# Kernel tuning notes

Hardware: AMD Instinct MI355X
Metric: run time of the kernel (lower is better)

## Reference

```python
import jax, jax.numpy as jnp
import numpy as np

LRELU = 0.2


def _gru(x, Wi, Wh, bi, bh):
    # x: [B,T,D]; Wi: [3H,D]; Wh: [3H,H]; PyTorch GRU equations.
    B, T, D = x.shape
    H = Wh.shape[1]
    xW = jnp.einsum('btd,gd->btg', x, Wi) + bi  # precompute input projections
    def step(h, xw):
        gh = h @ Wh.T + bh
        xr, xz, xn = jnp.split(xw, 3, axis=-1)
        hr, hz, hn = jnp.split(gh, 3, axis=-1)
        r = jax.nn.sigmoid(xr + hr)
        z = jax.nn.sigmoid(xz + hz)
        n = jnp.tanh(xn + r * hn)
        h_new = (1.0 - z) * n + z * h
        return h_new, h_new
    h0 = jnp.zeros((B, H), x.dtype)
    hT, hs = jax.lax.scan(step, h0, jnp.swapaxes(xW, 0, 1))
    return jnp.swapaxes(hs, 0, 1), hT


def _gatv2(x, W, b, a, bias):
    # x: [B,N,F]; W: [2F,E]; lin([v_i||v_j]) == x_i@W1 + x_j@W2 + b (avoids materializing concat)
    F = x.shape[-1]
    W1, W2 = W[:F], W[F:]
    g1 = x @ W1            # [B,N,E]
    g2 = x @ W2 + b        # [B,N,E]
    z = jax.nn.leaky_relu(g1[:, :, None, :] + g2[:, None, :, :], LRELU)  # [B,N,N,E]
    e = jnp.einsum('bije,e->bij', z, a) + bias
    att = jax.nn.softmax(e, axis=2)
    return jax.nn.sigmoid(jnp.einsum('bij,bjf->bif', att, x))


def setup_inputs() -> dict:
    B, W, K, H, KS = 16, 256, 64, 150, 7
    key = jax.random.key(0)
    ks = jax.random.split(key, 32)
    def rn(i, sh, scale):
        return jax.random.normal(ks[i], sh, jnp.float32) * scale
    inp = {}
    inp['x'] = jax.random.normal(ks[0], (B, W, K), jnp.float32)
    inp['conv_w'] = rn(1, (K, K, KS), 1.0 / np.sqrt(K * KS))
    inp['conv_b'] = rn(2, (K,), 0.02)
    inp['fW'] = rn(3, (2 * W, 2 * W), 1.0 / np.sqrt(2 * W))
    inp['fb'] = rn(4, (2 * W,), 0.02)
    inp['fa'] = rn(5, (2 * W,), 1.0 / np.sqrt(2 * W))
    inp['fbias'] = rn(6, (K, K), 0.02)
    inp['tW'] = rn(7, (2 * K, 2 * K), 1.0 / np.sqrt(2 * K))
    inp['tb'] = rn(8, (2 * K,), 0.02)
    inp['ta'] = rn(9, (2 * K,), 1.0 / np.sqrt(2 * K))
    inp['tbias'] = rn(10, (W, W), 0.02)
    inp['gWi'] = rn(11, (3 * H, 3 * K), 1.0 / np.sqrt(H))
    inp['gWh'] = rn(12, (3 * H, H), 1.0 / np.sqrt(H))
    inp['gbi'] = rn(13, (3 * H,), 0.02)
    inp['gbh'] = rn(14, (3 * H,), 0.02)
    inp['f0w'] = rn(15, (H, H), 1.0 / np.sqrt(H))
    inp['f0b'] = rn(16, (H,), 0.02)
    inp['f1w'] = rn(17, (H, K), 1.0 / np.sqrt(H))
    inp['f1b'] = rn(18, (K,), 0.02)
    inp['rWi'] = rn(19, (3 * H, H), 1.0 / np.sqrt(H))
    inp['rWh'] = rn(20, (3 * H, H), 1.0 / np.sqrt(H))
    inp['rbi'] = rn(21, (3 * H,), 0.02)
    inp['rbh'] = rn(22, (3 * H,), 0.02)
    inp['rfw'] = rn(23, (H, K), 1.0 / np.sqrt(H))
    inp['rfb'] = rn(24, (K,), 0.02)
    return inp


def reference(x, conv_w, conv_b, fW, fb, fa, fbias, tW, tb, ta, tbias,
              gWi, gWh, gbi, gbh, f0w, f0b, f1w, f1b,
              rWi, rWh, rbi, rbh, rfw, rfb):
    B, Wsz, K = x.shape
    pad = (conv_w.shape[2] - 1) // 2
    # ConvLayer: permute -> constant pad -> conv1d -> relu -> permute back
    x_ncw = jnp.swapaxes(x, 1, 2)  # [B,K,W]
    x_pad = jnp.pad(x_ncw, ((0, 0), (0, 0), (pad, pad)))
    xc = jax.lax.conv_general_dilated(x_pad, conv_w, (1,), 'VALID',
                                      dimension_numbers=('NCW', 'OIW', 'NCW'))
    xc = jax.nn.relu(xc + conv_b[None, :, None])
    xc = jnp.swapaxes(xc, 1, 2)  # [B,W,K]
    # Feature GAT over nodes (K), temporal GAT over time (W)
    h_feat = jnp.swapaxes(_gatv2(jnp.swapaxes(xc, 1, 2), fW, fb, fa, fbias), 1, 2)  # [B,W,K]
    h_temp = _gatv2(xc, tW, tb, ta, tbias)  # [B,W,K]
    h_cat = jnp.concatenate([xc, h_feat, h_temp], axis=2)  # [B,W,3K]
    _, h_end = _gru(h_cat, gWi, gWh, gbi, gbh)  # [B,H]
    # Forecasting MLP (n_layers=1 -> two Linear layers)
    predictions = jax.nn.relu(h_end @ f0w + f0b) @ f1w + f1b  # [B,K]
    # Reconstruction: repeat_interleave over dim 1 then view(B, W, -1)
    H = h_end.shape[1]
    h_rep = jnp.repeat(h_end, Wsz, axis=1).reshape(B, Wsz, H)
    dec_out, _ = _gru(h_rep, rWi, rWh, rbi, rbh)  # [B,W,H]
    recons = dec_out @ rfw + rfb  # [B,W,K]
    return predictions, recons
```

## Files before the change

### kernel.cpp

```cpp
#include <hip/hip_runtime.h>
#include <hip/hip_fp16.h>

typedef _Float16 h2f __attribute__((ext_vector_type(2)));

__device__ __forceinline__ float dot2f(unsigned a, unsigned b, float c) {
#if __has_builtin(__builtin_amdgcn_fdot2)
  return __builtin_amdgcn_fdot2(__builtin_bit_cast(h2f, a),
                                __builtin_bit_cast(h2f, b), c, false);
#else
  h2f x = __builtin_bit_cast(h2f, a);
  h2f y = __builtin_bit_cast(h2f, b);
  return c + (float)x[0] * (float)y[0] + (float)x[1] * (float)y[1];
#endif
}

template <int CTRL>
__device__ __forceinline__ float qxor_add(float v) {
  int r = __builtin_amdgcn_update_dpp(0, __builtin_bit_cast(int, v), CTRL, 0xF, 0xF, true);
  return v + __builtin_bit_cast(float, r);
}

__device__ __forceinline__ float sigf(float x) { return 1.0f / (1.0f + __expf(-x)); }
__device__ __forceinline__ float tanhfast(float x) {
  float e = __expf(-2.0f * fabsf(x));
  float r = (1.0f - e) / (1.0f + e);
  return (x < 0.0f) ? -r : r;
}
__device__ __forceinline__ float lrelu(float x) { return x > 0.0f ? x : 0.2f * x; }

__global__ void k_prep(const float* __restrict__ conv_w, const float* __restrict__ gWi,
                       const float* __restrict__ gWh, const float* __restrict__ rWh,
                       const float* __restrict__ rWi,
                       float* __restrict__ cwT, float* __restrict__ gWiT,
                       unsigned* __restrict__ gWhP, unsigned* __restrict__ rWhP,
                       float* __restrict__ pref) {
  const int N0 = 64 * 64 * 7;
  const int N1 = 192 * 450;
  const int N2 = 36000;
  const int N3 = 36000;
  const int N4 = 450;
  int total = N0 + N1 + N2 + N3 + N4;
  for (int idx = blockIdx.x * blockDim.x + threadIdx.x; idx < total;
       idx += gridDim.x * blockDim.x) {
    if (idx < N0) {
      int k = idx & 63; int is = idx >> 6; int i = is / 7; int s = is - i * 7;
      cwT[idx] = conv_w[(k * 64 + i) * 7 + s];
    } else if (idx < N0 + N1) {
      int j = idx - N0; int g = j % 450; int d = j / 450;
      gWiT[j] = gWi[g * 192 + d];
    } else if (idx < N0 + N1 + N2 + N3) {
      int u = idx - (N0 + N1);
      const float* W = gWh;
      unsigned* dst = gWhP;
      if (u >= N2) { u -= N2; W = rWh; dst = rWhP; }
      int c = u & 3; int q = u >> 2;
      int i = q / 600; int t6 = q - i * 600;
      int i2 = t6 >> 2, qt = t6 & 3;
      int gg = i / 5, li = i - gg * 5;
      int jj = qt * 20 + li * 4 + c;
      int e0 = 2 * jj, e1 = 2 * jj + 1;
      int row = i2 + gg * 150;
      float a = (e0 < 150) ? W[row * 150 + e0] : 0.f;
      float b = (e1 < 150) ? W[row * 150 + e1] : 0.f;
      __half2 h = __floats2half2_rn(a, b);
      dst[u] = *reinterpret_cast<unsigned*>(&h);
    } else {
      int g = idx - (N0 + N1 + N2 + N3);
      float run = 0.f;
      pref[g] = 0.f;
      for (int j = 0; j < 150; ++j) { run += rWi[g * 150 + j]; pref[(j + 1) * 450 + g] = run; }
    }
  }
}

__global__ __launch_bounds__(256) void k_conv(const float* __restrict__ x,
                                              const float* __restrict__ cwT,
                                              const float* __restrict__ conv_b,
                                              float* __restrict__ xc) {
  __shared__ float xs[22 * 64];
  int b = blockIdx.y, t0 = blockIdx.x * 16, tid = threadIdx.x;
  for (int l = tid; l < 22 * 64; l += 256) {
    int r = l >> 6, i = l & 63;
    int t = t0 - 3 + r;
    xs[l] = (t >= 0 && t < 256) ? x[(b * 256 + t) * 64 + i] : 0.f;
  }
  __syncthreads();
  int k = tid & 63, tg = tid >> 6;
  float bias = conv_b[k];
  float acc[4] = {bias, bias, bias, bias};
  for (int i = 0; i < 64; ++i) {
#pragma unroll
    for (int s = 0; s < 7; ++s) {
      float wv = cwT[(i * 7 + s) * 64 + k];
#pragma unroll
      for (int q = 0; q < 4; ++q)
        acc[q] += xs[(tg * 4 + q + s) * 64 + i] * wv;
    }
  }
#pragma unroll
  for (int q = 0; q < 4; ++q)
    xc[(b * 256 + t0 + tg * 4 + q) * 64 + k] = fmaxf(acc[q], 0.f);
}

__global__ __launch_bounds__(512) void k_featg(const float* __restrict__ xc,
                                               const float* __restrict__ fW,
                                               const float* __restrict__ fb,
                                               float* __restrict__ g1f,
                                               float* __restrict__ g2fT) {
  __shared__ float xsL[256 * 8];
  int b = blockIdx.y, i0 = blockIdx.x * 8, e = threadIdx.x;
  for (int l = e; l < 2048; l += 512) {
    int t = l >> 3, ii = l & 7;
    xsL[l] = xc[(b * 256 + t) * 64 + i0 + ii];
  }
  __syncthreads();
  float a1[8] = {}, a2[8] = {};
  for (int t = 0; t < 256; ++t) {
    float w1 = fW[t * 512 + e];
    float w2 = fW[(256 + t) * 512 + e];
#pragma unroll
    for (int ii = 0; ii < 8; ++ii) {
      float s = xsL[t * 8 + ii];
      a1[ii] += s * w1; a2[ii] += s * w2;
    }
  }
  float fbe = fb[e];
#pragma unroll
  for (int ii = 0; ii < 8; ++ii)
    g1f[(b * 64 + i0 + ii) * 512 + e] = a1[ii];
  float4 v0 = make_float4(a2[0] + fbe, a2[1] + fbe, a2[2] + fbe, a2[3] + fbe);
  float4 v1 = make_float4(a2[4] + fbe, a2[5] + fbe, a2[6] + fbe, a2[7] + fbe);
  float4* p = reinterpret_cast<float4*>(&g2fT[(b * 512 + e) * 64 + i0]);
  p[0] = v0; p[1] = v1;
}

__global__ __launch_bounds__(256) void k_feata(const float* __restrict__ xc,
                                               const float* __restrict__ g1f,
                                               const float* __restrict__ g2fT,
                                               const float* __restrict__ fa,
                                               const float* __restrict__ fbias,
                                               float* __restrict__ h_feat) {
  __shared__ float g1L[512], faL[512], part[4 * 64], attL[64];
  int b = blockIdx.y, i = blockIdx.x, tid = threadIdx.x;
  for (int l = tid; l < 512; l += 256) {
    g1L[l] = g1f[(b * 64 + i) * 512 + l];
    faL[l] = fa[l];
  }
  __syncthreads();
  int q = tid >> 6, j = tid & 63;
  float acc = 0.f;
  for (int e = q * 128; e < q * 128 + 128; ++e) {
    float z = g1L[e] + g2fT[(b * 512 + e) * 64 + j];
    acc += faL[e] * lrelu(z);
  }
  part[q * 64 + j] = acc;
  __syncthreads();
  if (tid < 64) {
    float ev = part[tid] + part[64 + tid] + part[128 + tid] + part[192 + tid] +
               fbias[i * 64 + tid];
    float m = ev;
#pragma unroll
    for (int off = 32; off > 0; off >>= 1) m = fmaxf(m, __shfl_xor(m, off));
    float p = __expf(ev - m);
    float s = p;
#pragma unroll
    for (int off = 32; off > 0; off >>= 1) s += __shfl_xor(s, off);
    attL[tid] = p / s;
  }
  __syncthreads();
  float o = 0.f;
  for (int jj = 0; jj < 64; ++jj)
    o += attL[jj] * xc[(b * 256 + tid) * 64 + jj];
  h_feat[(b * 256 + tid) * 64 + i] = sigf(o);
}

__global__ __launch_bounds__(256) void k_tempg(const float* __restrict__ xc,
                                               const float* __restrict__ tW,
                                               const float* __restrict__ tb,
                                               float* __restrict__ g1t,
                                               float* __restrict__ g2tT) {
  __shared__ float xsL[16 * 64];
  int b = blockIdx.y, t0 = blockIdx.x * 16, tid = threadIdx.x;
  int e = tid & 127, th = tid >> 7;
  for (int l = tid; l < 1024; l += 256)
    xsL[l] = xc[(b * 256 + t0) * 64 + l];
  __syncthreads();
  float a1[8] = {}, a2[8] = {};
  for (int k = 0; k < 64; ++k) {
    float w1 = tW[k * 128 + e];
    float w2 = tW[(64 + k) * 128 + e];
#pragma unroll
    for (int tt = 0; tt < 8; ++tt) {
      float s = xsL[(th * 8 + tt) * 64 + k];
      a1[tt] += s * w1; a2[tt] += s * w2;
    }
  }
  float tbe = tb[e];
#pragma unroll
  for (int tt = 0; tt < 8; ++tt)
    g1t[(b * 256 + t0 + th * 8 + tt) * 128 + e] = a1[tt];
  float4 v0 = make_float4(a2[0] + tbe, a2[1] + tbe, a2[2] + tbe, a2[3] + tbe);
  float4 v1 = make_float4(a2[4] + tbe, a2[5] + tbe, a2[6] + tbe, a2[7] + tbe);
  float4* p = reinterpret_cast<float4*>(&g2tT[(b * 128 + e) * 256 + t0 + th * 8]);
  p[0] = v0; p[1] = v1;
}

__global__ __launch_bounds__(256) void k_tempa(const float* __restrict__ xc,
                                               const float* __restrict__ g1t,
                                               const float* __restrict__ g2tT,
                                               const float* __restrict__ ta,
                                               const float* __restrict__ tbias,
                                               float* __restrict__ h_temp) {
  __shared__ float g1L[4 * 128], taL[128], eL[4 * 256];
  int b = blockIdx.y, i0 = blockIdx.x * 4, tid = threadIdx.x;
  for (int l = tid; l < 512; l += 256)
    g1L[l] = g1t[(b * 256 + i0) * 128 + l];
  if (tid < 128) taL[tid] = ta[tid];
  __syncthreads();
  float acc[4] = {};
  for (int e = 0; e < 128; ++e) {
    float g2 = g2tT[(b * 128 + e) * 256 + tid];
    float tae = taL[e];
#pragma unroll
    for (int ii = 0; ii < 4; ++ii)
      acc[ii] += tae * lrelu(g1L[ii * 128 + e] + g2);
  }
#pragma unroll
  for (int ii = 0; ii < 4; ++ii)
    eL[ii * 256 + tid] = acc[ii] + tbias[(i0 + ii) * 256 + tid];
  __syncthreads();
  int wv = tid >> 6, ln = tid & 63;
  {
    float v0 = eL[wv * 256 + ln], v1 = eL[wv * 256 + 64 + ln];
    float v2 = eL[wv * 256 + 128 + ln], v3 = eL[wv * 256 + 192 + ln];
    float m = fmaxf(fmaxf(v0, v1), fmaxf(v2, v3));
#pragma unroll
    for (int off = 32; off > 0; off >>= 1) m = fmaxf(m, __shfl_xor(m, off));
    float p0 = __expf(v0 - m), p1 = __expf(v1 - m);
    float p2 = __expf(v2 - m), p3 = __expf(v3 - m);
    float s = p0 + p1 + p2 + p3;
#pragma unroll
    for (int off = 32; off > 0; off >>= 1) s += __shfl_xor(s, off);
    float rs = 1.f / s;
    eL[wv * 256 + ln] = p0 * rs; eL[wv * 256 + 64 + ln] = p1 * rs;
    eL[wv * 256 + 128 + ln] = p2 * rs; eL[wv * 256 + 192 + ln] = p3 * rs;
  }
  __syncthreads();
  int ii = tid >> 6, k = tid & 63;
  float o = 0.f;
  for (int j = 0; j < 256; ++j)
    o += eL[ii * 256 + j] * xc[(b * 256 + j) * 64 + k];
  h_temp[(b * 256 + i0 + ii) * 64 + k] = sigf(o);
}

__global__ __launch_bounds__(256) void k_xw(const float* __restrict__ xc,
                                            const float* __restrict__ h_feat,
                                            const float* __restrict__ h_temp,
                                            const float* __restrict__ gWiT,
                                            const float* __restrict__ gbi,
                                            float* __restrict__ xW) {
  __shared__ float hc[16 * 192];
  int b = blockIdx.z, t0 = blockIdx.y * 16, g0 = blockIdx.x * 128;
  int tid = threadIdx.x;
  for (int l = tid; l < 16 * 192; l += 256) {
    int tt = l / 192, d = l - tt * 192;
    int row = (b * 256 + t0 + tt) * 64;
    float v;
    if (d < 64) v = xc[row + d];
    else if (d < 128) v = h_feat[row + d - 64];
    else v = h_temp[row + d - 128];
    hc[l] = v;
  }
  __syncthreads();
  int gl = tid & 127, th = tid >> 7;
  int g = g0 + gl;
  if (g < 450) {
    float acc[8] = {};
    for (int d = 0; d < 192; ++d) {
      float w = gWiT[d * 450 + g];
#pragma unroll
      for (int tt = 0; tt < 8; ++tt)
        acc[tt] += hc[(th * 8 + tt) * 192 + d] * w;
    }
    float bi = gbi[g];
#pragma unroll
    for (int tt = 0; tt < 8; ++tt)
      xW[(b * 256 + t0 + th * 8 + tt) * 450 + g] = acc[tt] + bi;
  }
}

#define D4(HH, WW, A, A2)            \
  A  = dot2f(HH.x, WW.x, A);         \
  A2 = dot2f(HH.y, WW.y, A2);        \
  A  = dot2f(HH.z, WW.z, A);         \
  A2 = dot2f(HH.w, WW.w, A2);

template <int MODE>
__global__ __launch_bounds__(640) void k_gru(const float* __restrict__ xwAll,
                                             const uint4* __restrict__ WhP4,
                                             const float* __restrict__ bh,
                                             const float* __restrict__ pref,
                                             const float* __restrict__ rbi,
                                             const float* __restrict__ h_end_in,
                                             float* __restrict__ h_end,
                                             float* __restrict__ dec_out) {
  __shared__ __align__(16) uint4 wlds[600 * 6];
  __shared__ __align__(16) uint4 hbuf[2][20];
  __shared__ float heL[152];
  int b = blockIdx.x, tid = threadIdx.x;
  bool act = tid < 600;
  int t6 = act ? tid : (tid - 600);
  int i2 = t6 >> 2, qt = t6 & 3;
  {
    unsigned* hz = reinterpret_cast<unsigned*>(&hbuf[0][0]);
    if (tid < 160) hz[tid] = 0u;
  }

  const uint4* Wp = WhP4 + t6;
  if (act) {
#pragma unroll
    for (int i = 0; i < 6; ++i) wlds[t6 * 6 + i] = Wp[i * 600];
  }

  float bhr = bh[i2], bhz = bh[i2 + 150], bhn = bh[i2 + 300];
  float bir = 0.f, biz = 0.f, bin_ = 0.f, totr = 0.f, totz = 0.f, totn = 0.f;
  if (MODE == 1) {
    if (tid < 152) heL[tid] = (tid < 150) ? h_end_in[b * 150 + tid] : 0.f;
    bir = rbi[i2]; biz = rbi[i2 + 150]; bin_ = rbi[i2 + 300];
    totr = pref[150 * 450 + i2];
    totz = pref[150 * 450 + i2 + 150];
    totn = pref[150 * 450 + i2 + 300];
  }
  const float* xwrow = xwAll ? (xwAll + (size_t)b * 256 * 450) : nullptr;

  auto ld3 = [&](int t, float& d0, float& d1, float& d2) {
    if (MODE == 0) {
      const float* p = xwrow + t * 450 + i2;
      d0 = p[0]; d1 = p[150]; d2 = p[300];
    } else {
      int base = 150 * t; int a = base >> 8;
      int c = 256 * (a + 1) - base; if (c > 150) c = 150;
      const float* p = pref + c * 450 + i2;
      d0 = p[0]; d1 = p[150]; d2 = p[300];
    }
  };

  float p0a, p0b, p0c;
  ld3(0, p0a, p0b, p0c);
  __syncthreads();

  float hprev = 0.f;
  __half* hout_base = reinterpret_cast<__half*>(&hbuf[0][0]);
#pragma unroll 2
  for (int t = 0; t < 256; ++t) {
    uint4 sz1 = Wp[6 * 600],  sz2 = Wp[7 * 600],  sz3 = Wp[8 * 600],
          sz4 = Wp[9 * 600];
    uint4 sn0 = Wp[10 * 600], sn1 = Wp[11 * 600], sn2 = Wp[12 * 600],
          sn3 = Wp[13 * 600], sn4 = Wp[14 * 600];

    float q0 = 0.f, q1 = 0.f, q2 = 0.f;
    if (t + 1 < 256) ld3(t + 1, q0, q1, q2);

    const uint4* wl = &wlds[t6 * 6];
    uint4 lr0 = wl[0], lr1 = wl[1], lr2 = wl[2], lr3 = wl[3], lr4 = wl[4];
    uint4 lz0 = wl[5];

    const uint4* hq = &hbuf[t & 1][qt * 5];
    uint4 h0 = hq[0], h1 = hq[1], h2 = hq[2], h3 = hq[3], h4 = hq[4];

    float ar = 0.f, ar2 = 0.f, az = 0.f, az2 = 0.f, an = 0.f, an2 = 0.f;
    D4(h0, lr0, ar, ar2) D4(h1, lr1, ar, ar2) D4(h2, lr2, ar, ar2)
    D4(h3, lr3, ar, ar2) D4(h4, lr4, ar, ar2)
    D4(h0, lz0, az, az2) D4(h1, sz1, az, az2) D4(h2, sz2, az, az2)
    D4(h3, sz3, az, az2) D4(h4, sz4, az, az2)
    D4(h0, sn0, an, an2) D4(h1, sn1, an, an2) D4(h2, sn2, an, an2)
    D4(h3, sn3, an, an2) D4(h4, sn4, an, an2)
    ar += ar2; az += az2; an += an2;
    ar = qxor_add<0xB1>(ar); ar = qxor_add<0x4E>(ar);
    az = qxor_add<0xB1>(az); az = qxor_add<0x4E>(az);
    an = qxor_add<0xB1>(an); an = qxor_add<0x4E>(an);
    ar += bhr; az += bhz; an += bhn;

    float xr, xz, xn;
    if (MODE == 0) {
      xr = p0a; xz = p0b; xn = p0c;
    } else {
      int base = 150 * t; int a = base >> 8;
      float hA = heL[a], hB = heL[a + 1];
      xr = bir + hA * p0a + hB * (totr - p0a);
      xz = biz + hA * p0b + hB * (totz - p0b);
      xn = bin_ + hA * p0c + hB * (totn - p0c);
    }
    float r = sigf(xr + ar);
    float z = sigf(xz + az);
    float n = tanhfast(xn + r * an);
    float hn = (1.f - z) * n + z * hprev;
    hprev = hn;
    if (act && qt == 0) {
      hout_base[((t & 1) ^ 1) * 160 + i2] = __float2half(hn);
      if (MODE == 1) dec_out[((size_t)(b * 256) + t) * 150 + i2] = hn;
    }
    p0a = q0; p0b = q1; p0c = q2;
    __syncthreads();
  }
  if (MODE == 0 && act && qt == 0) h_end[b * 150 + i2] = hprev;
}

__global__ __launch_bounds__(192) void k_pred(const float* __restrict__ h_end,
                                              const float* __restrict__ f0w,
                                              const float* __restrict__ f0b,
                                              const float* __restrict__ f1w,
                                              const float* __restrict__ f1b,
                                              float* __restrict__ out) {
  __shared__ float heL[152], t1L[152];
  int b = blockIdx.x, tid = threadIdx.x;
  if (tid < 152) heL[tid] = (tid < 150) ? h_end[b * 150 + tid] : 0.f;
  __syncthreads();
  if (tid < 150) {
    float a = f0b[tid];
    for (int i = 0; i < 150; ++i) a += heL[i] * f0w[i * 150 + tid];
    t1L[tid] = fmaxf(a, 0.f);
  }
  if (tid >= 150 && tid < 152) t1L[tid] = 0.f;
  __syncthreads();
  if (tid < 64) {
    float a = f1b[tid];
    for (int j = 0; j < 150; ++j) a += t1L[j] * f1w[j * 64 + tid];
    out[b * 64 + tid] = a;
  }
}

__global__ __launch_bounds__(256) void k_recon(const float* __restrict__ dec_out,
                                               const float* __restrict__ rfw,
                                               const float* __restrict__ rfb,
                                               float* __restrict__ out) {
  int row = blockIdx.x * 4 + (threadIdx.x >> 6);
  int k = threadIdx.x & 63;
  const float* d = dec_out + (size_t)row * 150;
  float a = rfb[k];
  for (int j = 0; j < 150; ++j) a += d[j] * rfw[j * 64 + k];
  out[1024 + (size_t)row * 64 + k] = a;
}

extern "C" void kernel_launch(void* const* d_in, const int* in_sizes, int n_in,
                              void* d_out, int out_size, void* d_ws, size_t ws_size,
                              hipStream_t stream) {
  (void)in_sizes; (void)n_in; (void)out_size; (void)ws_size;
  const float* x      = (const float*)d_in[0];
  const float* conv_w = (const float*)d_in[1];
  const float* conv_b = (const float*)d_in[2];
  const float* fW     = (const float*)d_in[3];
  const float* fb     = (const float*)d_in[4];
  const float* fa     = (const float*)d_in[5];
  const float* fbias  = (const float*)d_in[6];
  const float* tW     = (const float*)d_in[7];
  const float* tb     = (const float*)d_in[8];
  const float* ta     = (const float*)d_in[9];
  const float* tbias  = (const float*)d_in[10];
  const float* gWi    = (const float*)d_in[11];
  const float* gWh    = (const float*)d_in[12];
  const float* gbi    = (const float*)d_in[13];
  const float* gbh    = (const float*)d_in[14];
  const float* f0w    = (const float*)d_in[15];
  const float* f0b    = (const float*)d_in[16];
  const float* f1w    = (const float*)d_in[17];
  const float* f1b    = (const float*)d_in[18];
  const float* rWi    = (const float*)d_in[19];
  const float* rWh    = (const float*)d_in[20];
  const float* rbi    = (const float*)d_in[21];
  const float* rbh    = (const float*)d_in[22];
  const float* rfw    = (const float*)d_in[23];
  const float* rfb    = (const float*)d_in[24];
  float* out = (float*)d_out;
  float* ws  = (float*)d_ws;

  float* XC   = ws;
  float* HF   = XC + 262144;
  float* HT   = HF + 262144;
  float* GBUF = HT + 262144;
  float* G1F  = GBUF;
  float* G2FT = GBUF + 524288;
  float* G1T  = GBUF + 1048576;
  float* G2TT = GBUF + 1572864;
  float* XW   = GBUF;
  float* HEND = GBUF + 2097152;
  float* DEC  = HEND + 2400;
  float* CWT  = DEC + 614400;
  float* GWIT = CWT + 28672;
  unsigned* GWHP = (unsigned*)(GWIT + 86400);
  unsigned* RWHP = GWHP + 36000;
  float* PREF = (float*)(RWHP + 36000);

  k_prep<<<512, 256, 0, stream>>>(conv_w, gWi, gWh, rWh, rWi, CWT, GWIT, GWHP, RWHP, PREF);
  k_conv<<<dim3(16, 16), 256, 0, stream>>>(x, CWT, conv_b, XC);
  k_featg<<<dim3(8, 16), 512, 0, stream>>>(XC, fW, fb, G1F, G2FT);
  k_tempg<<<dim3(16, 16), 256, 0, stream>>>(XC, tW, tb, G1T, G2TT);
  k_feata<<<dim3(64, 16), 256, 0, stream>>>(XC, G1F, G2FT, fa, fbias, HF);
  k_tempa<<<dim3(64, 16), 256, 0, stream>>>(XC, G1T, G2TT, ta, tbias, HT);
  k_xw<<<dim3(4, 16, 16), 256, 0, stream>>>(XC, HF, HT, GWIT, gbi, XW);
  k_gru<0><<<16, 640, 0, stream>>>(XW, (const uint4*)GWHP, gbh, nullptr, nullptr, nullptr, HEND, nullptr);
  k_pred<<<16, 192, 0, stream>>>(HEND, f0w, f0b, f1w, f1b, out);
  k_gru<1><<<16, 640, 0, stream>>>(nullptr, (const uint4*)RWHP, rbh, PREF, rbi, HEND, nullptr, DEC);
  k_recon<<<1024, 256, 0, stream>>>(DEC, rfw, rfb, out);
}
```

Measured before the change: 762.9 us.

## Keep GRU recurrent weights resident in AccVGPRs instead of LDS and global reloads

The recurrent weight slices for all three gates are loaded once into accumulation VGPRs through inline asm, then read back into VGPRs each timestep for the dot products. Before, six of the fifteen uint4 slices came from LDS and nine were reloaded from global/L2 on every step. This removes that per-step memory traffic and frees the LDS array. It adds 60 accvgpr reads per step, and with 640 threads per block the register budget is tight.

```diff
diff --git a/kernel.cpp b/kernel.cpp
--- a/kernel.cpp
+++ b/kernel.cpp
@@ -289,11 +289,18 @@
   }
 }
 
-#define D4(HH, WW, A, A2)            \
-  A  = dot2f(HH.x, WW.x, A);         \
-  A2 = dot2f(HH.y, WW.y, A2);        \
-  A  = dot2f(HH.z, WW.z, A);         \
-  A2 = dot2f(HH.w, WW.w, A2);
+#define AW(A, V) asm volatile("v_accvgpr_write_b32 %0, %1" : "=a"(A) : "v"(V))
+#define AR(V, A) asm volatile("v_accvgpr_read_b32 %0, %1" : "=v"(V) : "a"(A))
+#define STASH4(Q, V) AW(Q.x, V.x); AW(Q.y, V.y); AW(Q.z, V.z); AW(Q.w, V.w)
+#define D4A(Q, HH, A, A2)                                             \
+  {                                                                   \
+    uint4 tw_;                                                        \
+    AR(tw_.x, Q.x); AR(tw_.y, Q.y); AR(tw_.z, Q.z); AR(tw_.w, Q.w);   \
+    A  = dot2f(HH.x, tw_.x, A);                                       \
+    A2 = dot2f(HH.y, tw_.y, A2);                                      \
+    A  = dot2f(HH.z, tw_.z, A);                                       \
+    A2 = dot2f(HH.w, tw_.w, A2);                                      \
+  }
 
 template <int MODE>
 __global__ __launch_bounds__(640) void k_gru(const float* __restrict__ xwAll,
@@ -304,7 +311,6 @@
                                              const float* __restrict__ h_end_in,
                                              float* __restrict__ h_end,
                                              float* __restrict__ dec_out) {
-  __shared__ __align__(16) uint4 wlds[600 * 6];
   __shared__ __align__(16) uint4 hbuf[2][20];
   __shared__ float heL[152];
   int b = blockIdx.x, tid = threadIdx.x;
@@ -317,9 +323,24 @@
   }
 
   const uint4* Wp = WhP4 + t6;
-  if (act) {
-#pragma unroll
-    for (int i = 0; i < 6; ++i) wlds[t6 * 6 + i] = Wp[i * 600];
+  uint4 qr0, qr1, qr2, qr3, qr4, qz0, qz1, qz2, qz3, qz4, qn0, qn1, qn2, qn3, qn4;
+  {
+    uint4 v;
+    v = Wp[0 * 600];  STASH4(qr0, v);
+    v = Wp[1 * 600];  STASH4(qr1, v);
+    v = Wp[2 * 600];  STASH4(qr2, v);
+    v = Wp[3 * 600];  STASH4(qr3, v);
+    v = Wp[4 * 600];  STASH4(qr4, v);
+    v = Wp[5 * 600];  STASH4(qz0, v);
+    v = Wp[6 * 600];  STASH4(qz1, v);
+    v = Wp[7 * 600];  STASH4(qz2, v);
+    v = Wp[8 * 600];  STASH4(qz3, v);
+    v = Wp[9 * 600];  STASH4(qz4, v);
+    v = Wp[10 * 600]; STASH4(qn0, v);
+    v = Wp[11 * 600]; STASH4(qn1, v);
+    v = Wp[12 * 600]; STASH4(qn2, v);
+    v = Wp[13 * 600]; STASH4(qn3, v);
+    v = Wp[14 * 600]; STASH4(qn4, v);
   }
 
   float bhr = bh[i2], bhz = bh[i2 + 150], bhn = bh[i2 + 300];
@@ -353,28 +374,19 @@
   __half* hout_base = reinterpret_cast<__half*>(&hbuf[0][0]);
 #pragma unroll 2
   for (int t = 0; t < 256; ++t) {
-    uint4 sz1 = Wp[6 * 600],  sz2 = Wp[7 * 600],  sz3 = Wp[8 * 600],
-          sz4 = Wp[9 * 600];
-    uint4 sn0 = Wp[10 * 600], sn1 = Wp[11 * 600], sn2 = Wp[12 * 600],
-          sn3 = Wp[13 * 600], sn4 = Wp[14 * 600];
-
     float q0 = 0.f, q1 = 0.f, q2 = 0.f;
     if (t + 1 < 256) ld3(t + 1, q0, q1, q2);
 
-    const uint4* wl = &wlds[t6 * 6];
-    uint4 lr0 = wl[0], lr1 = wl[1], lr2 = wl[2], lr3 = wl[3], lr4 = wl[4];
-    uint4 lz0 = wl[5];
-
     const uint4* hq = &hbuf[t & 1][qt * 5];
     uint4 h0 = hq[0], h1 = hq[1], h2 = hq[2], h3 = hq[3], h4 = hq[4];
 
     float ar = 0.f, ar2 = 0.f, az = 0.f, az2 = 0.f, an = 0.f, an2 = 0.f;
-    D4(h0, lr0, ar, ar2) D4(h1, lr1, ar, ar2) D4(h2, lr2, ar, ar2)
-    D4(h3, lr3, ar, ar2) D4(h4, lr4, ar, ar2)
-    D4(h0, lz0, az, az2) D4(h1, sz1, az, az2) D4(h2, sz2, az, az2)
-    D4(h3, sz3, az, az2) D4(h4, sz4, az, az2)
-    D4(h0, sn0, an, an2) D4(h1, sn1, an, an2) D4(h2, sn2, an, an2)
-    D4(h3, sn3, an, an2) D4(h4, sn4, an, an2)
+    D4A(qr0, h0, ar, ar2) D4A(qr1, h1, ar, ar2) D4A(qr2, h2, ar, ar2)
+    D4A(qr3, h3, ar, ar2) D4A(qr4, h4, ar, ar2)
+    D4A(qz0, h0, az, az2) D4A(qz1, h1, az, az2) D4A(qz2, h2, az, az2)
+    D4A(qz3, h3, az, az2) D4A(qz4, h4, az, az2)
+    D4A(qn0, h0, an, an2) D4A(qn1, h1, an, an2) D4A(qn2, h2, an, an2)
+    D4A(qn3, h3, an, an2) D4A(qn4, h4, an, an2)
     ar += ar2; az += az2; an += an2;
     ar = qxor_add<0xB1>(ar); ar = qxor_add<0x4E>(ar);
     az = qxor_add<0xB1>(az); az = qxor_add<0x4E>(az);
```

Result: slower. 835.9 us (+9.6%).
